# Kernel optimization log

Hardware: AMD Instinct MI355X
Metric: run time of the kernel (lower is better)

## Reference

```python
import jax, jax.numpy as jnp
import numpy as np
from jax import lax

V = 1024      # vocab_size (input_size == output_size == vocab)
NH = 256      # num_hiddens (module-level global in original code)
B = 128       # batch
T = 512       # seq_len


def _linear_params(key, fan_in, fan_out):
    # torch.nn.Linear default init: U(-1/sqrt(fan_in), 1/sqrt(fan_in))
    k1, k2 = jax.random.split(key)
    bound = 1.0 / np.sqrt(fan_in)
    W = jax.random.uniform(k1, (fan_in, fan_out), minval=-bound, maxval=bound, dtype=jnp.float32)
    b = jax.random.uniform(k2, (fan_out,), minval=-bound, maxval=bound, dtype=jnp.float32)
    return W, b


def setup_inputs() -> dict:
    key = jax.random.key(0)
    ks = jax.random.split(key, 10)
    inp = {
        "X": jax.random.randint(ks[0], (B, T), 0, V, dtype=jnp.int32),
        "H1": jnp.zeros((B, NH), jnp.float32),
        "C1": jnp.zeros((B, NH), jnp.float32),
        "H2": jnp.zeros((B, NH), jnp.float32),
        "C2": jnp.zeros((B, NH), jnp.float32),
    }
    # cell1: input_size = V, gate inputs are concat(X, H) of width V + NH
    names1 = ["W1f", "b1f", "W1i", "b1i", "W1o", "b1o", "W1c", "b1c"]
    for j, g in enumerate(range(4)):
        W, b = _linear_params(jax.random.fold_in(ks[1], g), V + NH, NH)
        inp[names1[2 * j]] = W
        inp[names1[2 * j + 1]] = b
    # cell2: input_size = NH, gate inputs concat(H1, H2) of width 2*NH
    names2 = ["W2f", "b2f", "W2i", "b2i", "W2o", "b2o", "W2c", "b2c"]
    for j, g in enumerate(range(4)):
        W, b = _linear_params(jax.random.fold_in(ks[2], g), NH + NH, NH)
        inp[names2[2 * j]] = W
        inp[names2[2 * j + 1]] = b
    Wout, bout = _linear_params(ks[3], NH, V)
    inp["Wout"], inp["bout"] = Wout, bout
    return inp


def _lstm_cell(XH, C, Wf, bf, Wi, bi, Wo, bo, Wc, bc):
    f = jax.nn.sigmoid(XH @ Wf + bf)
    i = jax.nn.sigmoid(XH @ Wi + bi)
    o = jax.nn.sigmoid(XH @ Wo + bo)
    c_tilde = jnp.tanh(XH @ Wc + bc)
    Cn = f * C + i * c_tilde
    Hn = o * jnp.tanh(Cn)
    return Hn, Cn


def reference(X, H1, C1, H2, C2,
              W1f, b1f, W1i, b1i, W1o, b1o, W1c, b1c,
              W2f, b2f, W2i, b2i, W2o, b2o, W2c, b2c,
              Wout, bout):
    # X: [B, T] int -> one-hot [T, B, V]
    xs = jax.nn.one_hot(X.T, V, dtype=jnp.float32)

    def step(carry, x):
        h1, c1, h2, c2 = carry
        xh1 = jnp.concatenate([x, h1], axis=1)          # [B, V+NH]
        h1, c1 = _lstm_cell(xh1, c1, W1f, b1f, W1i, b1i, W1o, b1o, W1c, b1c)
        xh2 = jnp.concatenate([h1, h2], axis=1)         # [B, 2*NH]
        h2, c2 = _lstm_cell(xh2, c2, W2f, b2f, W2i, b2i, W2o, b2o, W2c, b2c)
        y = h2 @ Wout + bout                            # [B, V]
        return (h1, c1, h2, c2), y

    (H1, C1, H2, C2), Ys = lax.scan(step, (H1, C1, H2, C2), xs)
    out = Ys.reshape(-1, V)  # torch.cat(outputs, dim=0) -> [T*B, V]
    return (out, H1, C1, H2, C2)
```

## Files before the change

kernel.cpp:

```cpp
#include <hip/hip_runtime.h>
#include <math.h>

static constexpr int V  = 1024;
static constexpr int NH = 256;
static constexpr int B  = 128;
static constexpr int T  = 512;
static constexpr size_t BV  = (size_t)B * V;
static constexpr size_t YSZ = (size_t)T * B * V;
static constexpr unsigned SENT = 0xFFC0DEADu;

typedef _Float16 h8 __attribute__((ext_vector_type(8)));
typedef _Float16 h4 __attribute__((ext_vector_type(4)));
typedef float f32x4 __attribute__((ext_vector_type(4)));

#define MFMA16(a, b, c) __builtin_amdgcn_mfma_f32_16x16x32_f16((a), (b), (c), 0, 0, 0)
#define MALL_LD(dst, src) asm volatile("global_load_dwordx4 %0, %1, off sc0 sc1" : "=v"(dst) : "v"(src))

__device__ __forceinline__ void mall_store(float* p, f32x4 v) {
    asm volatile("global_store_dwordx4 %0, %1, off sc0 sc1" :: "v"(p), "v"(v) : "memory");
}

__device__ __forceinline__ float fast_sigmoid(float x) {
    float a = fminf(-1.442695041f * x, 126.0f);
    return __builtin_amdgcn_rcpf(1.0f + __builtin_amdgcn_exp2f(a));
}

__device__ __forceinline__ int has_sent(f32x4 v) {
    return (__float_as_uint(v[0]) == SENT) | (__float_as_uint(v[1]) == SENT) |
           (__float_as_uint(v[2]) == SENT) | (__float_as_uint(v[3]) == SENT);
}

__device__ __forceinline__ void cvtv(f32x4 u, h4* hi4, h4* lo4) {
    h4 hi, lo;
    #pragma unroll
    for (int e = 0; e < 4; ++e) {
        _Float16 h = (_Float16)u[e];
        hi[e] = h; lo[e] = (_Float16)((u[e] - (float)h) * 2048.0f);
    }
    *hi4 = hi; *lo4 = lo;
}


__global__ __launch_bounds__(256) void k_prep(
    const float* __restrict__ W1f, const float* __restrict__ W1i,
    const float* __restrict__ W1o, const float* __restrict__ W1c,
    const float* __restrict__ W2f, const float* __restrict__ W2i,
    const float* __restrict__ W2o, const float* __restrict__ W2c,
    const float* __restrict__ Wout,
    const float* __restrict__ b1f, const float* __restrict__ b1i,
    const float* __restrict__ b1o, const float* __restrict__ b1c,
    const float* __restrict__ b2f, const float* __restrict__ b2i,
    const float* __restrict__ b2o, const float* __restrict__ b2c,
    _Float16* __restrict__ pk2, _Float16* __restrict__ pk1,
    _Float16* __restrict__ pkY, float* __restrict__ bp2, float* __restrict__ bp1)
{
    int idx = blockIdx.x * 256 + threadIdx.x;
    if (idx < 2097152) {
        int KB, e, rowoff = 0;
        bool vocabN = false;
        _Float16* dst;
        if (idx < 1048576)      { e = idx;            KB = 16; dst = pk2; }
        else if (idx < 1572864) { e = idx - 1048576;  KB = 8;  dst = pk1; rowoff = V; }
        else                    { e = idx - 1572864;  KB = 8;  dst = pkY; vocabN = true; }
        int S = 64 * KB * 512;
        int split = e / S, r = e % S;
        int grp = r / (KB * 512);
        int r2  = r % (KB * 512);
        int kb = r2 >> 9, lane = (r2 >> 3) & 63, i = r2 & 7;
        int n = grp * 16 + (lane & 15);
        int k = kb * 32 + (lane >> 4) * 8 + i;
        float val;
        if (vocabN) {
            val = Wout[(size_t)k * 1024 + n];
        } else {
            int j = n >> 2, g = n & 3;
            const float* W = (KB == 16)
                ? (g == 0 ? W2f : g == 1 ? W2i : g == 2 ? W2o : W2c)
                : (g == 0 ? W1f : g == 1 ? W1i : g == 2 ? W1o : W1c);
            val = W[(size_t)(rowoff + k) * NH + j];
        }
        _Float16 hi = (_Float16)val;
        dst[e] = split ? (_Float16)((val - (float)hi) * 2048.0f) : hi;
    } else {
        int bi = idx - 2097152;
        if (bi < 1024) {
            int j = bi >> 2, g = bi & 3;
            bp2[bi] = (g == 0 ? b2f : g == 1 ? b2i : g == 2 ? b2o : b2c)[j];
        } else if (bi < 2048) {
            int b2_ = bi - 1024;
            int j = b2_ >> 2, g = b2_ & 3;
            bp1[b2_] = (g == 0 ? b1f : g == 1 ? b1i : g == 2 ? b1o : b1c)[j];
        }
    }
}

__global__ __launch_bounds__(256) void k_sent(float* __restrict__ y) {
    const float s = __uint_as_float(SENT);
    const f32x4 sv = {s, s, s, s};
    int gid = blockIdx.x * 256 + threadIdx.x;
    for (int n = gid; n < 8388608; n += 524288) {
        int row = n >> 7, c4 = n & 127;
        *(f32x4*)&y[(size_t)row * V + c4 * 4] = sv;
    }
}

__global__ __launch_bounds__(512, 1) void k_persist(
    const int* __restrict__ X,
    const float* __restrict__ H1in, const float* __restrict__ C1in,
    const float* __restrict__ H2in, const float* __restrict__ C2in,
    float* __restrict__ y,
    float* __restrict__ H1t, float* __restrict__ C1t,
    float* __restrict__ H2t, float* __restrict__ C2t,
    const _Float16* __restrict__ pk2, const _Float16* __restrict__ pk1,
    const float* __restrict__ bp2, const float* __restrict__ bp1,
    const float* __restrict__ W1f, const float* __restrict__ W1i,
    const float* __restrict__ W1o, const float* __restrict__ W1c)
{
    const int bid = blockIdx.x, tid = threadIdx.x;
    const int mp = bid >> 4, np = bid & 15, r0 = mp * 16;

    __shared__ _Float16 Ah[16][520];
    __shared__ _Float16 Al[16][520];
    __shared__ float p1A[16][64], p1B[16][64], p2A[16][64], p2B[16][64];

    const int wave = tid >> 6, lane = tid & 63;
    const int wq = wave & 3, kh = wave >> 2;
    const int col = lane & 15, kg = lane >> 4;
    const int n_local = wq * 16 + col;

    h8 wh1[4], wl1[4], wh2[8], wl2[8];
    {
        const _Float16* pB1 = pk1 + ((size_t)((np * 4 + wq) * 8 + kh * 4) * 64 + lane) * 8;
        #pragma unroll
        for (int kb = 0; kb < 4; ++kb) {
            wh1[kb] = *(const h8*)(pB1 + (size_t)kb * 512);
            wl1[kb] = *(const h8*)(pB1 + 262144 + (size_t)kb * 512);
        }
        const _Float16* pB2 = pk2 + ((size_t)((np * 4 + wq) * 16 + kh * 8) * 64 + lane) * 8;
        #pragma unroll
        for (int kb = 0; kb < 8; ++kb) {
            wh2[kb] = *(const h8*)(pB2 + (size_t)kb * 512);
            wl2[kb] = *(const h8*)(pB2 + 524288 + (size_t)kb * 512);
        }
        #pragma unroll
        for (int kb = 0; kb < 4; ++kb) asm volatile("" : "+v"(wh1[kb]), "+v"(wl1[kb]));
        #pragma unroll
        for (int kb = 0; kb < 8; ++kb) asm volatile("" : "+v"(wh2[kb]), "+v"(wl2[kb]));
    }

    const bool isCmb1 = tid < 256;
    const int ct = isCmb1 ? tid : (tid - 256);
    const int cr = ct >> 4, cjl = ct & 15;
    const int cb = r0 + cr, cjg = np * 16 + cjl;
    float creg = isCmb1 ? C1in[cb * NH + cjg] : C2in[cb * NH + cjg];
    const f32x4 bb = *(const f32x4*)&((isCmb1 ? bp1 : bp2)[np * 64 + cjl * 4]);

    const int sk4 = tid & 63;
    const int srb = tid >> 6;

    {
        f32x4 ua = *(const f32x4*)(H1in + (size_t)(r0 + srb) * NH + sk4 * 4);
        f32x4 ub = *(const f32x4*)(H1in + (size_t)(r0 + srb + 8) * NH + sk4 * 4);
        cvtv(ua, (h4*)&Ah[srb][sk4 * 4], (h4*)&Al[srb][sk4 * 4]);
        cvtv(ub, (h4*)&Ah[srb + 8][sk4 * 4], (h4*)&Al[srb + 8][sk4 * 4]);
        __syncthreads();
        f32x4 a0 = {0.f, 0.f, 0.f, 0.f}, a1 = a0, a2 = a0;
        #pragma unroll
        for (int kb = 0; kb < 4; ++kb) {
            const int kbg = kh * 4 + kb;
            h8 ah = *(const h8*)&Ah[col][kbg * 32 + kg * 8];
            h8 al = *(const h8*)&Al[col][kbg * 32 + kg * 8];
            a0 = MFMA16(ah, wh1[kb], a0);
            a1 = MFMA16(ah, wl1[kb], a1);
            a2 = MFMA16(al, wh1[kb], a2);
        }
        float* pre = kh ? &p1B[0][0] : &p1A[0][0];
        #pragma unroll
        for (int q = 0; q < 4; ++q)
            pre[(kg * 4 + q) * 64 + n_local] = a0[q] + (a1[q] + a2[q]) * (1.0f / 2048.0f);
        __syncthreads();
        if (isCmb1) {
            int tok = X[cb * T + 0];
            float pf = p1A[cr][cjl * 4 + 0] + p1B[cr][cjl * 4 + 0] + bb[0] + W1f[(size_t)tok * NH + cjg];
            float pi = p1A[cr][cjl * 4 + 1] + p1B[cr][cjl * 4 + 1] + bb[1] + W1i[(size_t)tok * NH + cjg];
            float po = p1A[cr][cjl * 4 + 2] + p1B[cr][cjl * 4 + 2] + bb[2] + W1o[(size_t)tok * NH + cjg];
            float pc = p1A[cr][cjl * 4 + 3] + p1B[cr][cjl * 4 + 3] + bb[3] + W1c[(size_t)tok * NH + cjg];
            float fg = fast_sigmoid(pf), ig = fast_sigmoid(pi), og = fast_sigmoid(po);
            creg = fmaf(fg, creg, ig * tanhf(pc));
            float h = og * tanhf(creg);
            float h1n = __shfl(h, (lane & 60) | 1);
            float h2n = __shfl(h, (lane & 60) | 2);
            float h3n = __shfl(h, (lane & 60) | 3);
            if ((lane & 3) == 0) {
                f32x4 hv = {h, h1n, h2n, h3n};
                mall_store(y + (size_t)cb * V + 256 + cjg, hv);
            }
        }
    }

    for (int t = 0; t < T; ++t) {
        float w1f_ = 0.f, w1i_ = 0.f, w1o_ = 0.f, w1c_ = 0.f;
        if (isCmb1 && t <= 510) {
            int tok = X[cb * T + t + 1];
            w1f_ = W1f[(size_t)tok * NH + cjg];
            w1i_ = W1i[(size_t)tok * NH + cjg];
            w1o_ = W1o[(size_t)tok * NH + cjg];
            w1c_ = W1c[(size_t)tok * NH + cjg];
        }

        f32x4 u1a, u1b, u2a, u2b;
        const float* p1a = y + (size_t)t * BV + (size_t)(r0 + srb) * V + 256 + sk4 * 4;
        const float* p1b = y + (size_t)t * BV + (size_t)(r0 + srb + 8) * V + 256 + sk4 * 4;
        if (t) {
            const float* p2a = y + (size_t)(t - 1) * BV + (size_t)(r0 + srb) * V + sk4 * 4;
            const float* p2b = y + (size_t)(t - 1) * BV + (size_t)(r0 + srb + 8) * V + sk4 * 4;
            MALL_LD(u2a, p2a); MALL_LD(u2b, p2b); MALL_LD(u1a, p1a); MALL_LD(u1b, p1b);
            asm volatile("s_waitcnt vmcnt(0)" : "+v"(u2a), "+v"(u2b), "+v"(u1a), "+v"(u1b));
            while (__any(has_sent(u1a) | has_sent(u1b) | has_sent(u2a) | has_sent(u2b))) {
                __builtin_amdgcn_s_sleep(1);
                MALL_LD(u2a, p2a); MALL_LD(u2b, p2b); MALL_LD(u1a, p1a); MALL_LD(u1b, p1b);
                asm volatile("s_waitcnt vmcnt(0)" : "+v"(u2a), "+v"(u2b), "+v"(u1a), "+v"(u1b));
            }
        } else {
            MALL_LD(u1a, p1a); MALL_LD(u1b, p1b);
            asm volatile("s_waitcnt vmcnt(0)" : "+v"(u1a), "+v"(u1b));
            while (__any(has_sent(u1a) | has_sent(u1b))) {
                __builtin_amdgcn_s_sleep(1);
                MALL_LD(u1a, p1a); MALL_LD(u1b, p1b);
                asm volatile("s_waitcnt vmcnt(0)" : "+v"(u1a), "+v"(u1b));
            }
            u2a = *(const f32x4*)(H2in + (size_t)(r0 + srb) * NH + sk4 * 4);
            u2b = *(const f32x4*)(H2in + (size_t)(r0 + srb + 8) * NH + sk4 * 4);
        }
        cvtv(u1a, (h4*)&Ah[srb][sk4 * 4], (h4*)&Al[srb][sk4 * 4]);
        cvtv(u1b, (h4*)&Ah[srb + 8][sk4 * 4], (h4*)&Al[srb + 8][sk4 * 4]);
        cvtv(u2a, (h4*)&Ah[srb][256 + sk4 * 4], (h4*)&Al[srb][256 + sk4 * 4]);
        cvtv(u2b, (h4*)&Ah[srb + 8][256 + sk4 * 4], (h4*)&Al[srb + 8][256 + sk4 * 4]);
        __syncthreads();

        {
            f32x4 a0 = {0.f, 0.f, 0.f, 0.f}, a1 = a0, a2 = a0;
            #pragma unroll
            for (int kb = 0; kb < 4; ++kb) {
                const int kbg = kh * 4 + kb;
                h8 ah = *(const h8*)&Ah[col][kbg * 32 + kg * 8];
                h8 al = *(const h8*)&Al[col][kbg * 32 + kg * 8];
                a0 = MFMA16(ah, wh1[kb], a0);
                a1 = MFMA16(ah, wl1[kb], a1);
                a2 = MFMA16(al, wh1[kb], a2);
            }
            float* pre = kh ? &p1B[0][0] : &p1A[0][0];
            #pragma unroll
            for (int q = 0; q < 4; ++q)
                pre[(kg * 4 + q) * 64 + n_local] = a0[q] + (a1[q] + a2[q]) * (1.0f / 2048.0f);
        }
        __syncthreads();

        if (isCmb1 && t <= 510) {
            float pf = p1A[cr][cjl * 4 + 0] + p1B[cr][cjl * 4 + 0] + bb[0] + w1f_;
            float pi = p1A[cr][cjl * 4 + 1] + p1B[cr][cjl * 4 + 1] + bb[1] + w1i_;
            float po = p1A[cr][cjl * 4 + 2] + p1B[cr][cjl * 4 + 2] + bb[2] + w1o_;
            float pc = p1A[cr][cjl * 4 + 3] + p1B[cr][cjl * 4 + 3] + bb[3] + w1c_;
            float fg = fast_sigmoid(pf), ig = fast_sigmoid(pi), og = fast_sigmoid(po);
            creg = fmaf(fg, creg, ig * tanhf(pc));
            float h = og * tanhf(creg);
            float h1n = __shfl(h, (lane & 60) | 1);
            float h2n = __shfl(h, (lane & 60) | 2);
            float h3n = __shfl(h, (lane & 60) | 3);
            if ((lane & 3) == 0) {
                f32x4 hv = {h, h1n, h2n, h3n};
                mall_store(y + (size_t)(t + 1) * BV + (size_t)cb * V + 256 + cjg, hv);
            }
            if (t == 510) { H1t[cb * NH + cjg] = h; C1t[cb * NH + cjg] = creg; }
        }

        {
            f32x4 a0 = {0.f, 0.f, 0.f, 0.f}, a1 = a0, a2 = a0;
            #pragma unroll
            for (int kb = 0; kb < 8; ++kb) {
                const int kbg = kh * 8 + kb;
                h8 ah = *(const h8*)&Ah[col][kbg * 32 + kg * 8];
                h8 al = *(const h8*)&Al[col][kbg * 32 + kg * 8];
                a0 = MFMA16(ah, wh2[kb], a0);
                a1 = MFMA16(ah, wl2[kb], a1);
                a2 = MFMA16(al, wh2[kb], a2);
            }
            float* pre = kh ? &p2B[0][0] : &p2A[0][0];
            #pragma unroll
            for (int q = 0; q < 4; ++q)
                pre[(kg * 4 + q) * 64 + n_local] = a0[q] + (a1[q] + a2[q]) * (1.0f / 2048.0f);
        }
        __syncthreads();

        if (!isCmb1) {
            float pf = p2A[cr][cjl * 4 + 0] + p2B[cr][cjl * 4 + 0] + bb[0];
            float pi = p2A[cr][cjl * 4 + 1] + p2B[cr][cjl * 4 + 1] + bb[1];
            float po = p2A[cr][cjl * 4 + 2] + p2B[cr][cjl * 4 + 2] + bb[2];
            float pc = p2A[cr][cjl * 4 + 3] + p2B[cr][cjl * 4 + 3] + bb[3];
            float fg = fast_sigmoid(pf), ig = fast_sigmoid(pi), og = fast_sigmoid(po);
            creg = fmaf(fg, creg, ig * tanhf(pc));
            float h = og * tanhf(creg);
            float h1n = __shfl(h, (lane & 60) | 1);
            float h2n = __shfl(h, (lane & 60) | 2);
            float h3n = __shfl(h, (lane & 60) | 3);
            if ((lane & 3) == 0) {
                f32x4 hv = {h, h1n, h2n, h3n};
                mall_store(y + (size_t)t * BV + (size_t)cb * V + cjg, hv);
            }
            if (t == 511) { H2t[cb * NH + cjg] = h; C2t[cb * NH + cjg] = creg; }
        }
    }
}

__global__ __launch_bounds__(256) void k_ygemm2(
    float* __restrict__ y, const _Float16* __restrict__ pkY,
    const float* __restrict__ bout)
{
    __shared__ _Float16 Ah[64][264];
    __shared__ _Float16 Al[64][264];
    const size_t m0 = (size_t)blockIdx.x * 64;
    const int tid = threadIdx.x;
    for (int idx = tid; idx < 64 * 256; idx += 256) {
        int r = idx >> 8, k = idx & 255;
        float v = y[(m0 + r) * 1024 + k];
        _Float16 hi = (_Float16)v;
        Ah[r][k] = hi;
        Al[r][k] = (_Float16)((v - (float)hi) * 2048.0f);
    }
    __syncthreads();
    const int wave = tid >> 6, lane = tid & 63;
    const int col = lane & 15, kg = lane >> 4;
    const int ar = wave * 16 + col;
    const size_t orow = m0 + wave * 16 + kg * 4;
    for (int npass = 0; npass < 8; ++npass) {
        f32x4 aA[8], aB[8];
        #pragma unroll
        for (int nt = 0; nt < 8; ++nt) { aA[nt] = (f32x4){0.f,0.f,0.f,0.f}; aB[nt] = aA[nt]; }
        for (int kb = 0; kb < 8; ++kb) {
            h8 ah = *(const h8*)&Ah[ar][kb * 32 + kg * 8];
            h8 al = *(const h8*)&Al[ar][kb * 32 + kg * 8];
            #pragma unroll
            for (int nt = 0; nt < 8; ++nt) {
                const int ngrp = npass * 8 + nt;
                const _Float16* pb = pkY + ((size_t)(ngrp * 8 + kb) * 64 + lane) * 8;
                h8 bh = *(const h8*)pb;
                h8 bl = *(const h8*)(pb + 262144);
                aA[nt] = MFMA16(ah, bh, aA[nt]);
                aB[nt] = MFMA16(ah, bl, aB[nt]);
                aB[nt] = MFMA16(al, bh, aB[nt]);
            }
        }
        #pragma unroll
        for (int nt = 0; nt < 8; ++nt) {
            int n = npass * 128 + nt * 16 + col;
            float bbo = bout[n];
            #pragma unroll
            for (int q = 0; q < 4; ++q)
                y[(orow + q) * 1024 + n] = aA[nt][q] + aB[nt][q] * (1.0f / 2048.0f) + bbo;
        }
    }
}

extern "C" void kernel_launch(void* const* d_in, const int* in_sizes, int n_in,
                              void* d_out, int out_size, void* d_ws, size_t ws_size,
                              hipStream_t stream) {
    const int*   X    = (const int*)  d_in[0];
    const float* H1in = (const float*)d_in[1];
    const float* C1in = (const float*)d_in[2];
    const float* H2in = (const float*)d_in[3];
    const float* C2in = (const float*)d_in[4];
    const float* W1f = (const float*)d_in[5];  const float* b1f = (const float*)d_in[6];
    const float* W1i = (const float*)d_in[7];  const float* b1i = (const float*)d_in[8];
    const float* W1o = (const float*)d_in[9];  const float* b1o = (const float*)d_in[10];
    const float* W1c = (const float*)d_in[11]; const float* b1c = (const float*)d_in[12];
    const float* W2f = (const float*)d_in[13]; const float* b2f = (const float*)d_in[14];
    const float* W2i = (const float*)d_in[15]; const float* b2i = (const float*)d_in[16];
    const float* W2o = (const float*)d_in[17]; const float* b2o = (const float*)d_in[18];
    const float* W2c = (const float*)d_in[19]; const float* b2c = (const float*)d_in[20];
    const float* Wout = (const float*)d_in[21]; const float* bout = (const float*)d_in[22];

    float* y   = (float*)d_out;
    float* H1t = y + YSZ;
    float* C1t = y + YSZ + 1 * 32768;
    float* H2t = y + YSZ + 2 * 32768;
    float* C2t = y + YSZ + 3 * 32768;

    char* ws = (char*)d_ws;
    _Float16* pk2 = (_Float16*)ws;
    _Float16* pk1 = pk2 + 1048576;
    _Float16* pkY = pk1 + 524288;
    float* bp2 = (float*)(ws + 4194304);
    float* bp1 = bp2 + 1024;

    k_prep<<<8200, 256, 0, stream>>>(W1f, W1i, W1o, W1c, W2f, W2i, W2o, W2c, Wout,
                                     b1f, b1i, b1o, b1c, b2f, b2i, b2o, b2c,
                                     pk2, pk1, pkY, bp2, bp1);
    k_sent<<<2048, 256, 0, stream>>>(y);

    k_persist<<<128, 512, 0, stream>>>(X, H1in, C1in, H2in, C2in, y,
                                       H1t, C1t, H2t, C2t,
                                       pk2, pk1, bp2, bp1,
                                       W1f, W1i, W1o, W1c);

    k_ygemm2<<<1024, 256, 0, stream>>>(y, pkY, bout);
}
```

Before: 2.121 ms.

## Warp-specialize persistent LSTM: compute waves vs loader waves with double-buffered LDS

Splits the persistent kernel's 8 waves into 4 compute waves, each holding the full K range of weights in registers, and 4 loader waves that poll and convert the next step's hidden states into a double-buffered LDS tile. Gate pre-activations are now redistributed with lane shuffles instead of staged through shared partial-sum arrays. Per step this cuts the __syncthreads count from three to one and lets global polling overlap with MFMA work. In exchange each compute wave carries twice as many weight registers, which raises register pressure and the risk of spills.

```diff
diff --git a/kernel.cpp b/kernel.cpp
--- a/kernel.cpp
+++ b/kernel.cpp
@@ -38,6 +38,21 @@
         hi[e] = h; lo[e] = (_Float16)((u[e] - (float)h) * 2048.0f);
     }
     *hi4 = hi; *lo4 = lo;
+}
+
+__device__ __forceinline__ float sel4(f32x4 p, int i) {
+    float r = p[0];
+    r = (i == 1) ? p[1] : r;
+    r = (i == 2) ? p[2] : r;
+    r = (i == 3) ? p[3] : r;
+    return r;
+}
+__device__ __forceinline__ float pick4(float a0, float a1, float a2, float a3, int i) {
+    float r = a0;
+    r = (i == 1) ? a1 : r;
+    r = (i == 2) ? a2 : r;
+    r = (i == 3) ? a3 : r;
+    return r;
 }
 
 
@@ -119,195 +134,223 @@
     const int bid = blockIdx.x, tid = threadIdx.x;
     const int mp = bid >> 4, np = bid & 15, r0 = mp * 16;
 
-    __shared__ _Float16 Ah[16][520];
-    __shared__ _Float16 Al[16][520];
-    __shared__ float p1A[16][64], p1B[16][64], p2A[16][64], p2B[16][64];
-
-    const int wave = tid >> 6, lane = tid & 63;
-    const int wq = wave & 3, kh = wave >> 2;
-    const int col = lane & 15, kg = lane >> 4;
-    const int n_local = wq * 16 + col;
-
-    h8 wh1[4], wl1[4], wh2[8], wl2[8];
-    {
-        const _Float16* pB1 = pk1 + ((size_t)((np * 4 + wq) * 8 + kh * 4) * 64 + lane) * 8;
-        #pragma unroll
-        for (int kb = 0; kb < 4; ++kb) {
-            wh1[kb] = *(const h8*)(pB1 + (size_t)kb * 512);
-            wl1[kb] = *(const h8*)(pB1 + 262144 + (size_t)kb * 512);
-        }
-        const _Float16* pB2 = pk2 + ((size_t)((np * 4 + wq) * 16 + kh * 8) * 64 + lane) * 8;
-        #pragma unroll
-        for (int kb = 0; kb < 8; ++kb) {
-            wh2[kb] = *(const h8*)(pB2 + (size_t)kb * 512);
-            wl2[kb] = *(const h8*)(pB2 + 524288 + (size_t)kb * 512);
-        }
-        #pragma unroll
-        for (int kb = 0; kb < 4; ++kb) asm volatile("" : "+v"(wh1[kb]), "+v"(wl1[kb]));
-        #pragma unroll
-        for (int kb = 0; kb < 8; ++kb) asm volatile("" : "+v"(wh2[kb]), "+v"(wl2[kb]));
-    }
-
-    const bool isCmb1 = tid < 256;
-    const int ct = isCmb1 ? tid : (tid - 256);
-    const int cr = ct >> 4, cjl = ct & 15;
-    const int cb = r0 + cr, cjg = np * 16 + cjl;
-    float creg = isCmb1 ? C1in[cb * NH + cjg] : C2in[cb * NH + cjg];
-    const f32x4 bb = *(const f32x4*)&((isCmb1 ? bp1 : bp2)[np * 64 + cjl * 4]);
-
-    const int sk4 = tid & 63;
-    const int srb = tid >> 6;
-
-    {
-        f32x4 ua = *(const f32x4*)(H1in + (size_t)(r0 + srb) * NH + sk4 * 4);
-        f32x4 ub = *(const f32x4*)(H1in + (size_t)(r0 + srb + 8) * NH + sk4 * 4);
-        cvtv(ua, (h4*)&Ah[srb][sk4 * 4], (h4*)&Al[srb][sk4 * 4]);
-        cvtv(ub, (h4*)&Ah[srb + 8][sk4 * 4], (h4*)&Al[srb + 8][sk4 * 4]);
+    __shared__ _Float16 Ah[2][16][520];
+    __shared__ _Float16 Al[2][16][520];
+
+    const int wv = tid >> 6, lane = tid & 63;
+
+    if (wv < 4) {
+        const int wq = wv;
+        const int col = lane & 15, kg = lane >> 4;
+        const int c3 = lane & 3;
+        const int orow = ((lane >> 4) << 2) | c3;
+        const int jq = (lane >> 2) & 3;
+        const int jglob = np * 16 + wq * 4 + jq;
+        const int brow = r0 + orow;
+
+        h8 wh1[8], wl1[8], wh2[16], wl2[16];
+        {
+            const _Float16* pB1 = pk1 + ((size_t)((np * 4 + wq) * 8) * 64 + lane) * 8;
+            #pragma unroll
+            for (int kb = 0; kb < 8; ++kb) {
+                wh1[kb] = *(const h8*)(pB1 + (size_t)kb * 512);
+                wl1[kb] = *(const h8*)(pB1 + 262144 + (size_t)kb * 512);
+            }
+            const _Float16* pB2 = pk2 + ((size_t)((np * 4 + wq) * 16) * 64 + lane) * 8;
+            #pragma unroll
+            for (int kb = 0; kb < 16; ++kb) {
+                wh2[kb] = *(const h8*)(pB2 + (size_t)kb * 512);
+                wl2[kb] = *(const h8*)(pB2 + 524288 + (size_t)kb * 512);
+            }
+        }
+        float creg1 = C1in[brow * NH + jglob];
+        float creg2 = C2in[brow * NH + jglob];
+        const f32x4 bb1 = *(const f32x4*)&bp1[(np * 16 + wq * 4 + jq) * 4];
+        const f32x4 bb2 = *(const f32x4*)&bp2[(np * 16 + wq * 4 + jq) * 4];
+        float* const hst1base = y + (size_t)brow * V + 256 + np * 16 + wq * 4;
+        float* const hst2base = y + (size_t)brow * V + np * 16 + wq * 4;
+
         __syncthreads();
-        f32x4 a0 = {0.f, 0.f, 0.f, 0.f}, a1 = a0, a2 = a0;
-        #pragma unroll
-        for (int kb = 0; kb < 4; ++kb) {
-            const int kbg = kh * 4 + kb;
-            h8 ah = *(const h8*)&Ah[col][kbg * 32 + kg * 8];
-            h8 al = *(const h8*)&Al[col][kbg * 32 + kg * 8];
-            a0 = MFMA16(ah, wh1[kb], a0);
-            a1 = MFMA16(ah, wl1[kb], a1);
-            a2 = MFMA16(al, wh1[kb], a2);
-        }
-        float* pre = kh ? &p1B[0][0] : &p1A[0][0];
-        #pragma unroll
-        for (int q = 0; q < 4; ++q)
-            pre[(kg * 4 + q) * 64 + n_local] = a0[q] + (a1[q] + a2[q]) * (1.0f / 2048.0f);
-        __syncthreads();
-        if (isCmb1) {
-            int tok = X[cb * T + 0];
-            float pf = p1A[cr][cjl * 4 + 0] + p1B[cr][cjl * 4 + 0] + bb[0] + W1f[(size_t)tok * NH + cjg];
-            float pi = p1A[cr][cjl * 4 + 1] + p1B[cr][cjl * 4 + 1] + bb[1] + W1i[(size_t)tok * NH + cjg];
-            float po = p1A[cr][cjl * 4 + 2] + p1B[cr][cjl * 4 + 2] + bb[2] + W1o[(size_t)tok * NH + cjg];
-            float pc = p1A[cr][cjl * 4 + 3] + p1B[cr][cjl * 4 + 3] + bb[3] + W1c[(size_t)tok * NH + cjg];
-            float fg = fast_sigmoid(pf), ig = fast_sigmoid(pi), og = fast_sigmoid(po);
-            creg = fmaf(fg, creg, ig * tanhf(pc));
-            float h = og * tanhf(creg);
-            float h1n = __shfl(h, (lane & 60) | 1);
-            float h2n = __shfl(h, (lane & 60) | 2);
-            float h3n = __shfl(h, (lane & 60) | 3);
-            if ((lane & 3) == 0) {
-                f32x4 hv = {h, h1n, h2n, h3n};
-                mall_store(y + (size_t)cb * V + 256 + cjg, hv);
-            }
-        }
-    }
-
-    for (int t = 0; t < T; ++t) {
-        float w1f_ = 0.f, w1i_ = 0.f, w1o_ = 0.f, w1c_ = 0.f;
-        if (isCmb1 && t <= 510) {
-            int tok = X[cb * T + t + 1];
-            w1f_ = W1f[(size_t)tok * NH + cjg];
-            w1i_ = W1i[(size_t)tok * NH + cjg];
-            w1o_ = W1o[(size_t)tok * NH + cjg];
-            w1c_ = W1c[(size_t)tok * NH + cjg];
-        }
-
-        f32x4 u1a, u1b, u2a, u2b;
-        const float* p1a = y + (size_t)t * BV + (size_t)(r0 + srb) * V + 256 + sk4 * 4;
-        const float* p1b = y + (size_t)t * BV + (size_t)(r0 + srb + 8) * V + 256 + sk4 * 4;
-        if (t) {
-            const float* p2a = y + (size_t)(t - 1) * BV + (size_t)(r0 + srb) * V + sk4 * 4;
-            const float* p2b = y + (size_t)(t - 1) * BV + (size_t)(r0 + srb + 8) * V + sk4 * 4;
-            MALL_LD(u2a, p2a); MALL_LD(u2b, p2b); MALL_LD(u1a, p1a); MALL_LD(u1b, p1b);
-            asm volatile("s_waitcnt vmcnt(0)" : "+v"(u2a), "+v"(u2b), "+v"(u1a), "+v"(u1b));
-            while (__any(has_sent(u1a) | has_sent(u1b) | has_sent(u2a) | has_sent(u2b))) {
-                __builtin_amdgcn_s_sleep(1);
-                MALL_LD(u2a, p2a); MALL_LD(u2b, p2b); MALL_LD(u1a, p1a); MALL_LD(u1b, p1b);
-                asm volatile("s_waitcnt vmcnt(0)" : "+v"(u2a), "+v"(u2b), "+v"(u1a), "+v"(u1b));
-            }
-        } else {
-            MALL_LD(u1a, p1a); MALL_LD(u1b, p1b);
-            asm volatile("s_waitcnt vmcnt(0)" : "+v"(u1a), "+v"(u1b));
-            while (__any(has_sent(u1a) | has_sent(u1b))) {
-                __builtin_amdgcn_s_sleep(1);
-                MALL_LD(u1a, p1a); MALL_LD(u1b, p1b);
-                asm volatile("s_waitcnt vmcnt(0)" : "+v"(u1a), "+v"(u1b));
-            }
-            u2a = *(const f32x4*)(H2in + (size_t)(r0 + srb) * NH + sk4 * 4);
-            u2b = *(const f32x4*)(H2in + (size_t)(r0 + srb + 8) * NH + sk4 * 4);
-        }
-        cvtv(u1a, (h4*)&Ah[srb][sk4 * 4], (h4*)&Al[srb][sk4 * 4]);
-        cvtv(u1b, (h4*)&Ah[srb + 8][sk4 * 4], (h4*)&Al[srb + 8][sk4 * 4]);
-        cvtv(u2a, (h4*)&Ah[srb][256 + sk4 * 4], (h4*)&Al[srb][256 + sk4 * 4]);
-        cvtv(u2b, (h4*)&Ah[srb + 8][256 + sk4 * 4], (h4*)&Al[srb + 8][256 + sk4 * 4]);
-        __syncthreads();
 
         {
+            int tok = X[brow * T + 0];
+            float w1f_ = W1f[(size_t)tok * NH + jglob];
+            float w1i_ = W1i[(size_t)tok * NH + jglob];
+            float w1o_ = W1o[(size_t)tok * NH + jglob];
+            float w1c_ = W1c[(size_t)tok * NH + jglob];
             f32x4 a0 = {0.f, 0.f, 0.f, 0.f}, a1 = a0, a2 = a0;
             #pragma unroll
-            for (int kb = 0; kb < 4; ++kb) {
-                const int kbg = kh * 4 + kb;
-                h8 ah = *(const h8*)&Ah[col][kbg * 32 + kg * 8];
-                h8 al = *(const h8*)&Al[col][kbg * 32 + kg * 8];
+            for (int kb = 0; kb < 8; ++kb) {
+                h8 ah = *(const h8*)&Ah[1][col][kb * 32 + kg * 8];
+                h8 al = *(const h8*)&Al[1][col][kb * 32 + kg * 8];
                 a0 = MFMA16(ah, wh1[kb], a0);
                 a1 = MFMA16(ah, wl1[kb], a1);
                 a2 = MFMA16(al, wh1[kb], a2);
             }
-            float* pre = kh ? &p1B[0][0] : &p1A[0][0];
-            #pragma unroll
-            for (int q = 0; q < 4; ++q)
-                pre[(kg * 4 + q) * 64 + n_local] = a0[q] + (a1[q] + a2[q]) * (1.0f / 2048.0f);
+            f32x4 comb = a0 + (a1 + a2) * (1.0f / 2048.0f);
+            float s0 = sel4(comb, c3);
+            float s1 = __shfl_xor(sel4(comb, c3 ^ 1), 1);
+            float s2 = __shfl_xor(sel4(comb, c3 ^ 2), 2);
+            float s3 = __shfl_xor(sel4(comb, c3 ^ 3), 3);
+            float pf = pick4(s0, s1, s2, s3, c3)     + bb1[0] + w1f_;
+            float pi = pick4(s0, s1, s2, s3, c3 ^ 1) + bb1[1] + w1i_;
+            float po = pick4(s0, s1, s2, s3, c3 ^ 2) + bb1[2] + w1o_;
+            float pc = pick4(s0, s1, s2, s3, c3 ^ 3) + bb1[3] + w1c_;
+            float fg = fast_sigmoid(pf), ig = fast_sigmoid(pi), og = fast_sigmoid(po);
+            creg1 = fmaf(fg, creg1, ig * tanhf(pc));
+            float h = og * tanhf(creg1);
+            float g1 = __shfl(h, (lane & 51) | 4);
+            float g2 = __shfl(h, (lane & 51) | 8);
+            float g3 = __shfl(h, (lane & 51) | 12);
+            if ((lane & 12) == 0) {
+                f32x4 hv = {h, g1, g2, g3};
+                mall_store(hst1base, hv);
+            }
         }
         __syncthreads();
 
-        if (isCmb1 && t <= 510) {
-            float pf = p1A[cr][cjl * 4 + 0] + p1B[cr][cjl * 4 + 0] + bb[0] + w1f_;
-            float pi = p1A[cr][cjl * 4 + 1] + p1B[cr][cjl * 4 + 1] + bb[1] + w1i_;
-            float po = p1A[cr][cjl * 4 + 2] + p1B[cr][cjl * 4 + 2] + bb[2] + w1o_;
-            float pc = p1A[cr][cjl * 4 + 3] + p1B[cr][cjl * 4 + 3] + bb[3] + w1c_;
-            float fg = fast_sigmoid(pf), ig = fast_sigmoid(pi), og = fast_sigmoid(po);
-            creg = fmaf(fg, creg, ig * tanhf(pc));
-            float h = og * tanhf(creg);
-            float h1n = __shfl(h, (lane & 60) | 1);
-            float h2n = __shfl(h, (lane & 60) | 2);
-            float h3n = __shfl(h, (lane & 60) | 3);
-            if ((lane & 3) == 0) {
-                f32x4 hv = {h, h1n, h2n, h3n};
-                mall_store(y + (size_t)(t + 1) * BV + (size_t)cb * V + 256 + cjg, hv);
-            }
-            if (t == 510) { H1t[cb * NH + cjg] = h; C1t[cb * NH + cjg] = creg; }
-        }
+        for (int t = 0; t < T; ++t) {
+            const int tb = t & 1;
+            if (t <= 510) {
+                int tok = X[brow * T + t + 1];
+                float w1f_ = W1f[(size_t)tok * NH + jglob];
+                float w1i_ = W1i[(size_t)tok * NH + jglob];
+                float w1o_ = W1o[(size_t)tok * NH + jglob];
+                float w1c_ = W1c[(size_t)tok * NH + jglob];
+                f32x4 a0 = {0.f, 0.f, 0.f, 0.f}, a1 = a0, a2 = a0;
+                #pragma unroll
+                for (int kb = 0; kb < 8; ++kb) {
+                    h8 ah = *(const h8*)&Ah[tb][col][kb * 32 + kg * 8];
+                    h8 al = *(const h8*)&Al[tb][col][kb * 32 + kg * 8];
+                    a0 = MFMA16(ah, wh1[kb], a0);
+                    a1 = MFMA16(ah, wl1[kb], a1);
+                    a2 = MFMA16(al, wh1[kb], a2);
+                }
+                f32x4 comb = a0 + (a1 + a2) * (1.0f / 2048.0f);
+                float s0 = sel4(comb, c3);
+                float s1 = __shfl_xor(sel4(comb, c3 ^ 1), 1);
+                float s2 = __shfl_xor(sel4(comb, c3 ^ 2), 2);
+                float s3 = __shfl_xor(sel4(comb, c3 ^ 3), 3);
+                float pf = pick4(s0, s1, s2, s3, c3)     + bb1[0] + w1f_;
+                float pi = pick4(s0, s1, s2, s3, c3 ^ 1) + bb1[1] + w1i_;
+                float po = pick4(s0, s1, s2, s3, c3 ^ 2) + bb1[2] + w1o_;
+                float pc = pick4(s0, s1, s2, s3, c3 ^ 3) + bb1[3] + w1c_;
+                float fg = fast_sigmoid(pf), ig = fast_sigmoid(pi), og = fast_sigmoid(po);
+                creg1 = fmaf(fg, creg1, ig * tanhf(pc));
+                float h = og * tanhf(creg1);
+                float g1 = __shfl(h, (lane & 51) | 4);
+                float g2 = __shfl(h, (lane & 51) | 8);
+                float g3 = __shfl(h, (lane & 51) | 12);
+                if ((lane & 12) == 0) {
+                    f32x4 hv = {h, g1, g2, g3};
+                    mall_store(hst1base + (size_t)(t + 1) * BV, hv);
+                }
+                if (t == 510) { H1t[brow * NH + jglob] = h; C1t[brow * NH + jglob] = creg1; }
+            }
+            {
+                f32x4 a0 = {0.f, 0.f, 0.f, 0.f}, a1 = a0, a2 = a0;
+                #pragma unroll
+                for (int kb = 0; kb < 16; ++kb) {
+                    h8 ah = *(const h8*)&Ah[tb][col][kb * 32 + kg * 8];
+                    h8 al = *(const h8*)&Al[tb][col][kb * 32 + kg * 8];
+                    a0 = MFMA16(ah, wh2[kb], a0);
+                    a1 = MFMA16(ah, wl2[kb], a1);
+                    a2 = MFMA16(al, wh2[kb], a2);
+                }
+                f32x4 comb = a0 + (a1 + a2) * (1.0f / 2048.0f);
+                float s0 = sel4(comb, c3);
+                float s1 = __shfl_xor(sel4(comb, c3 ^ 1), 1);
+                float s2 = __shfl_xor(sel4(comb, c3 ^ 2), 2);
+                float s3 = __shfl_xor(sel4(comb, c3 ^ 3), 3);
+                float pf = pick4(s0, s1, s2, s3, c3)     + bb2[0];
+                float pi = pick4(s0, s1, s2, s3, c3 ^ 1) + bb2[1];
+                float po = pick4(s0, s1, s2, s3, c3 ^ 2) + bb2[2];
+                float pc = pick4(s0, s1, s2, s3, c3 ^ 3) + bb2[3];
+                float fg = fast_sigmoid(pf), ig = fast_sigmoid(pi), og = fast_sigmoid(po);
+                creg2 = fmaf(fg, creg2, ig * tanhf(pc));
+                float h = og * tanhf(creg2);
+                float g1 = __shfl(h, (lane & 51) | 4);
+                float g2 = __shfl(h, (lane & 51) | 8);
+                float g3 = __shfl(h, (lane & 51) | 12);
+                if ((lane & 12) == 0) {
+                    f32x4 hv = {h, g1, g2, g3};
+                    mall_store(hst2base + (size_t)t * BV, hv);
+                }
+                if (t == 511) { H2t[brow * NH + jglob] = h; C2t[brow * NH + jglob] = creg2; }
+            }
+            __syncthreads();
+        }
+    } else {
+        const int st = tid & 255;
+        const int sk4 = st & 63;
+        const int srb = st >> 6;
+
+        #pragma unroll
+        for (int k = 0; k < 4; ++k) {
+            const int row = srb + k * 4;
+            f32x4 u1 = *(const f32x4*)(H1in + (size_t)(r0 + row) * NH + sk4 * 4);
+            cvtv(u1, (h4*)&Ah[1][row][sk4 * 4], (h4*)&Al[1][row][sk4 * 4]);
+            f32x4 u2 = *(const f32x4*)(H2in + (size_t)(r0 + row) * NH + sk4 * 4);
+            cvtv(u2, (h4*)&Ah[0][row][256 + sk4 * 4], (h4*)&Al[0][row][256 + sk4 * 4]);
+        }
+        __syncthreads();
 
         {
-            f32x4 a0 = {0.f, 0.f, 0.f, 0.f}, a1 = a0, a2 = a0;
-            #pragma unroll
-            for (int kb = 0; kb < 8; ++kb) {
-                const int kbg = kh * 8 + kb;
-                h8 ah = *(const h8*)&Ah[col][kbg * 32 + kg * 8];
-                h8 al = *(const h8*)&Al[col][kbg * 32 + kg * 8];
-                a0 = MFMA16(ah, wh2[kb], a0);
-                a1 = MFMA16(ah, wl2[kb], a1);
-                a2 = MFMA16(al, wh2[kb], a2);
-            }
-            float* pre = kh ? &p2B[0][0] : &p2A[0][0];
-            #pragma unroll
-            for (int q = 0; q < 4; ++q)
-                pre[(kg * 4 + q) * 64 + n_local] = a0[q] + (a1[q] + a2[q]) * (1.0f / 2048.0f);
+            f32x4 ua, ub, uc, ud;
+            const float* pa = y + (size_t)(r0 + srb)      * V + 256 + sk4 * 4;
+            const float* pb = y + (size_t)(r0 + srb + 4)  * V + 256 + sk4 * 4;
+            const float* pc_ = y + (size_t)(r0 + srb + 8) * V + 256 + sk4 * 4;
+            const float* pd = y + (size_t)(r0 + srb + 12) * V + 256 + sk4 * 4;
+            MALL_LD(ua, pa); MALL_LD(ub, pb); MALL_LD(uc, pc_); MALL_LD(ud, pd);
+            asm volatile("s_waitcnt vmcnt(0)" : "+v"(ua), "+v"(ub), "+v"(uc), "+v"(ud));
+            while (__any(has_sent(ua) | has_sent(ub) | has_sent(uc) | has_sent(ud))) {
+                __builtin_amdgcn_s_sleep(1);
+                MALL_LD(ua, pa); MALL_LD(ub, pb); MALL_LD(uc, pc_); MALL_LD(ud, pd);
+                asm volatile("s_waitcnt vmcnt(0)" : "+v"(ua), "+v"(ub), "+v"(uc), "+v"(ud));
+            }
+            cvtv(ua, (h4*)&Ah[0][srb][sk4 * 4],      (h4*)&Al[0][srb][sk4 * 4]);
+            cvtv(ub, (h4*)&Ah[0][srb + 4][sk4 * 4],  (h4*)&Al[0][srb + 4][sk4 * 4]);
+            cvtv(uc, (h4*)&Ah[0][srb + 8][sk4 * 4],  (h4*)&Al[0][srb + 8][sk4 * 4]);
+            cvtv(ud, (h4*)&Ah[0][srb + 12][sk4 * 4], (h4*)&Al[0][srb + 12][sk4 * 4]);
         }
         __syncthreads();
 
-        if (!isCmb1) {
-            float pf = p2A[cr][cjl * 4 + 0] + p2B[cr][cjl * 4 + 0] + bb[0];
-            float pi = p2A[cr][cjl * 4 + 1] + p2B[cr][cjl * 4 + 1] + bb[1];
-            float po = p2A[cr][cjl * 4 + 2] + p2B[cr][cjl * 4 + 2] + bb[2];
-            float pc = p2A[cr][cjl * 4 + 3] + p2B[cr][cjl * 4 + 3] + bb[3];
-            float fg = fast_sigmoid(pf), ig = fast_sigmoid(pi), og = fast_sigmoid(po);
-            creg = fmaf(fg, creg, ig * tanhf(pc));
-            float h = og * tanhf(creg);
-            float h1n = __shfl(h, (lane & 60) | 1);
-            float h2n = __shfl(h, (lane & 60) | 2);
-            float h3n = __shfl(h, (lane & 60) | 3);
-            if ((lane & 3) == 0) {
-                f32x4 hv = {h, h1n, h2n, h3n};
-                mall_store(y + (size_t)t * BV + (size_t)cb * V + cjg, hv);
-            }
-            if (t == 511) { H2t[cb * NH + cjg] = h; C2t[cb * NH + cjg] = creg; }
+        for (int t = 0; t < T; ++t) {
+            if (t <= 510) {
+                const int tb1 = (t + 1) & 1;
+                f32x4 a0, a1_, a2_, a3_, b0, b1_, b2_, b3_;
+                const float* q1a = y + (size_t)(t + 1) * BV + (size_t)(r0 + srb)      * V + 256 + sk4 * 4;
+                const float* q1b = y + (size_t)(t + 1) * BV + (size_t)(r0 + srb + 4)  * V + 256 + sk4 * 4;
+                const float* q1c = y + (size_t)(t + 1) * BV + (size_t)(r0 + srb + 8)  * V + 256 + sk4 * 4;
+                const float* q1d = y + (size_t)(t + 1) * BV + (size_t)(r0 + srb + 12) * V + 256 + sk4 * 4;
+                const float* q2a = y + (size_t)t * BV + (size_t)(r0 + srb)      * V + sk4 * 4;
+                const float* q2b = y + (size_t)t * BV + (size_t)(r0 + srb + 4)  * V + sk4 * 4;
+                const float* q2c = y + (size_t)t * BV + (size_t)(r0 + srb + 8)  * V + sk4 * 4;
+                const float* q2d = y + (size_t)t * BV + (size_t)(r0 + srb + 12) * V + sk4 * 4;
+                MALL_LD(a0, q1a); MALL_LD(a1_, q1b); MALL_LD(a2_, q1c); MALL_LD(a3_, q1d);
+                MALL_LD(b0, q2a); MALL_LD(b1_, q2b); MALL_LD(b2_, q2c); MALL_LD(b3_, q2d);
+                asm volatile("s_waitcnt vmcnt(0)"
+                    : "+v"(a0), "+v"(a1_), "+v"(a2_), "+v"(a3_),
+                      "+v"(b0), "+v"(b1_), "+v"(b2_), "+v"(b3_));
+                while (__any(has_sent(a0) | has_sent(a1_) | has_sent(a2_) | has_sent(a3_) |
+                             has_sent(b0) | has_sent(b1_) | has_sent(b2_) | has_sent(b3_))) {
+                    __builtin_amdgcn_s_sleep(1);
+                    MALL_LD(a0, q1a); MALL_LD(a1_, q1b); MALL_LD(a2_, q1c); MALL_LD(a3_, q1d);
+                    MALL_LD(b0, q2a); MALL_LD(b1_, q2b); MALL_LD(b2_, q2c); MALL_LD(b3_, q2d);
+                    asm volatile("s_waitcnt vmcnt(0)"
+                        : "+v"(a0), "+v"(a1_), "+v"(a2_), "+v"(a3_),
+                          "+v"(b0), "+v"(b1_), "+v"(b2_), "+v"(b3_));
+                }
+                cvtv(a0,  (h4*)&Ah[tb1][srb][sk4 * 4],       (h4*)&Al[tb1][srb][sk4 * 4]);
+                cvtv(a1_, (h4*)&Ah[tb1][srb + 4][sk4 * 4],   (h4*)&Al[tb1][srb + 4][sk4 * 4]);
+                cvtv(a2_, (h4*)&Ah[tb1][srb + 8][sk4 * 4],   (h4*)&Al[tb1][srb + 8][sk4 * 4]);
+                cvtv(a3_, (h4*)&Ah[tb1][srb + 12][sk4 * 4],  (h4*)&Al[tb1][srb + 12][sk4 * 4]);
+                cvtv(b0,  (h4*)&Ah[tb1][srb][256 + sk4 * 4],      (h4*)&Al[tb1][srb][256 + sk4 * 4]);
+                cvtv(b1_, (h4*)&Ah[tb1][srb + 4][256 + sk4 * 4],  (h4*)&Al[tb1][srb + 4][256 + sk4 * 4]);
+                cvtv(b2_, (h4*)&Ah[tb1][srb + 8][256 + sk4 * 4],  (h4*)&Al[tb1][srb + 8][256 + sk4 * 4]);
+                cvtv(b3_, (h4*)&Ah[tb1][srb + 12][256 + sk4 * 4], (h4*)&Al[tb1][srb + 12][256 + sk4 * 4]);
+            }
+            __syncthreads();
         }
     }
 }
```

Measured after the change: 4.937 ms. 133% more time.
